# Performance work log

Measured on AMD Instinct MI355X. Metric: run time of the kernel, lower is better.

The kernel has to match this reference:

```python
import jax, jax.numpy as jnp
from jax import lax
import numpy as np

B, N, J, NI, D = 2, 2048, 24, 9, 3
CD, HID = 16, 128
SOFT_BLEND = 20.0
MAX_STEPS, CVG = 50, 1e-5
INIT_BONES = np.array([0, 1, 2, 4, 5, 16, 17, 18, 19])


def _mlp(params, x):
    h = x
    for W, b in params[:-1]:
        h = jax.nn.softplus(h @ W + b)
    W, b = params[-1]
    return h @ W + b


def _broyden(g, x0, J_inv0):
    # x0: [P,3,1], J_inv0: [P,3,3]; fixed MAX_STEPS iterations, track best iterate
    gx = g(x0)
    err0 = jnp.linalg.norm(gx, axis=(1, 2))
    state = (x0, gx, J_inv0, -(J_inv0 @ gx), x0, err0)

    def body(i, st):
        x, gx, Jinv, upd, bx, berr = st
        dx = upd
        x = x + dx
        gx_new = g(x)
        dgx = gx_new - gx
        vT = jnp.swapaxes(dx, -2, -1) @ Jinv            # [P,1,3]
        a = dx - Jinv @ dgx                              # [P,3,1]
        b = vT @ dgx + 1e-6                              # [P,1,1]
        Jinv = Jinv + (a / b) @ vT                       # rank-1 Broyden update
        upd = -(Jinv @ gx_new)
        err = jnp.linalg.norm(gx_new, axis=(1, 2))
        better = err < berr
        bx = jnp.where(better[:, None, None], x, bx)
        berr = jnp.where(better, err, berr)
        return (x, gx_new, Jinv, upd, bx, berr)

    st = lax.fori_loop(0, MAX_STEPS, body, state)
    return st[4], st[5] < CVG


def setup_inputs():
    key = jax.random.key(0)
    ks = jax.random.split(key, 24)
    xd = 0.5 * jax.random.normal(ks[0], (B, N, D), jnp.float32)
    cond_latent = jax.random.normal(ks[1], (B, CD), jnp.float32)
    # near-identity invertible bone transforms
    R = jnp.eye(3, dtype=jnp.float32) + 0.1 * jax.random.normal(ks[2], (B, J, 3, 3), jnp.float32)
    t = 0.1 * jax.random.normal(ks[3], (B, J, 3), jnp.float32)
    tfs = jnp.zeros((B, J, 4, 4), jnp.float32)
    tfs = tfs.at[..., :3, :3].set(R).at[..., :3, 3].set(t).at[..., 3, 3].set(1.0)

    def w(k, fi, fo):
        return jax.random.normal(k, (fi, fo), jnp.float32) / np.sqrt(fi)

    din = D + CD
    inp = dict(xd=xd, cond_latent=cond_latent, tfs=tfs)
    dims_lbs = [(din, HID), (HID, HID), (HID, HID), (HID, J)]
    dims_disp = [(din, HID), (HID, HID), (HID, HID), (HID, D)]
    for i, (fi, fo) in enumerate(dims_lbs):
        inp[f"lbs_w{i}"] = w(ks[4 + i], fi, fo)
        inp[f"lbs_b{i}"] = jnp.zeros((fo,), jnp.float32)
    for i, (fi, fo) in enumerate(dims_disp):
        inp[f"disp_w{i}"] = w(ks[10 + i], fi, fo)
        inp[f"disp_b{i}"] = jnp.zeros((fo,), jnp.float32)
    return inp


def _forward(xd, cond_latent, tfs, lbs, disp):
    P = B * N
    xd_f = xd.reshape(P, D)
    cond_f = jnp.broadcast_to(cond_latent[:, None], (B, N, CD)).reshape(P, CD)
    tfs_f = jnp.broadcast_to(tfs[:, None], (B, N, J, 4, 4)).reshape(P, J, 4, 4)

    # __init: inverse-skin xd with one-hot weights at each init bone -> [P, NI, 3]
    xd_h = jnp.concatenate([xd_f, jnp.ones((P, 1), xd.dtype)], -1)
    xc_init = jnp.einsum('pnij,pj->pni', jnp.linalg.inv(tfs_f[:, INIT_BONES]), xd_h)[..., :3]

    PI = P * NI
    cond_e = jnp.repeat(cond_f, NI, axis=0)       # [PI, CD]
    tfs_e = jnp.repeat(tfs_f, NI, axis=0)         # [PI, J, 4, 4]
    xd_tgt = jnp.repeat(xd_f, NI, axis=0)         # [PI, 3]
    x0 = xc_init.reshape(PI, D)

    def fwd_skin(xc, lbs_p, cond_p, tfs_p):
        w = jax.nn.softmax(SOFT_BLEND * _mlp(lbs_p, jnp.concatenate([xc, cond_p], -1)), -1)
        xh = jnp.concatenate([xc, jnp.ones_like(xc[:, :1])], -1)
        return jnp.einsum('pn,pnij,pj->pi', w, tfs_p, xh)[:, :3]

    def fwd_skin_pt(x, c, t, lbs_p):
        w = jax.nn.softmax(SOFT_BLEND * _mlp(lbs_p, jnp.concatenate([x, c])))
        xh = jnp.concatenate([x, jnp.ones((1,), x.dtype)])
        return jnp.einsum('n,nij,j->i', w, t, xh)[:3]

    def gradient(xc, lbs_p, cond_p, tfs_p):
        # per-point 3x3 Jacobian of forward skinning wrt canonical point
        f = lambda x, c, t: fwd_skin_pt(x, c, t, lbs_p)
        return jax.vmap(jax.jacfwd(f), in_axes=(0, 0, 0))(xc, cond_p, tfs_p)

    # stop-gradient copies for the no-grad broyden search (torch.no_grad block)
    sg = lax.stop_gradient
    lbs_sg = [(sg(W), sg(b)) for W, b in lbs]
    cond_sg, tfs_sg, xdt_sg = sg(cond_e), sg(tfs_e), sg(xd_tgt)

    J_inv0 = jnp.linalg.inv(gradient(sg(x0), lbs_sg, cond_sg, tfs_sg))

    def g_ng(x):  # x: [PI,3,1]
        return (fwd_skin(x[..., 0], lbs_sg, cond_sg, tfs_sg) - xdt_sg)[..., None]

    x_opt, valid = _broyden(g_ng, sg(x0)[..., None], J_inv0)
    xc_opt = sg(x_opt[..., 0])

    # implicit-differentiation correction (eval_mode=False path)
    xd_opt = fwd_skin(xc_opt, lbs, cond_e, tfs_e)
    grad_inv = jnp.linalg.inv(gradient(xc_opt, lbs, cond_e, tfs_e))
    corr = jnp.einsum('pij,pj->pi', -sg(grad_inv), xd_opt - sg(xd_opt))
    xc = xc_opt + corr

    # __query_cano: beta displacement network
    xc = xc + _mlp(disp, jnp.concatenate([xc, cond_e], -1))
    return xc.reshape(B, N, NI, D), valid.reshape(B, N, NI)


def reference(xd, cond_latent, tfs, lbs_w0, lbs_b0, lbs_w1, lbs_b1, lbs_w2, lbs_b2, lbs_w3, lbs_b3, disp_w0, disp_b0, disp_w1, disp_b1, disp_w2, disp_b2, disp_w3, disp_b3):
    lbs = [(lbs_w0, lbs_b0), (lbs_w1, lbs_b1), (lbs_w2, lbs_b2), (lbs_w3, lbs_b3)]
    disp = [(disp_w0, disp_b0), (disp_w1, disp_b1), (disp_w2, disp_b2), (disp_w3, disp_b3)]
    return _forward(xd, cond_latent, tfs, lbs, disp)
```

## Files before the change

### kernel.cpp

```cpp
#include <hip/hip_runtime.h>
#include <math.h>

#define NB 2
#define NN 2048
#define NJ 24
#define NIB 9
#define NCD 16
#define NHID 128
#define NP (NB * NN)
#define NPI (NP * NIB)
#define NBSTRIDE (NN * NIB)
#define SBLEND 20.0f
#define CVG_EPS 1e-5f
#define MAX_STEPS 50
#define N_A 12

#define HSTR 129
#define INSTRD 21
#define LSTR 25

#define WS_BX 4
#define WS_BE (4 + 3 * NPI)
#define WS_META (4 + 4 * NPI)
#define WS_ST (4 + 5 * NPI)

static __device__ __forceinline__ float softplusf(float x) {
    return fmaxf(x, 0.0f) + log1pf(expf(-fabsf(x)));
}
static __device__ __forceinline__ float sigmoidf(float x) {
    return 1.0f / (1.0f + expf(-x));
}
static __device__ __forceinline__ int bone_of(int ib) {
    return (ib < 3) ? ib : ((ib < 5) ? ib + 1 : ib + 11);
}

template <int K>
static __device__ __forceinline__ void mv_acc16(const float* __restrict__ Wp, const float* inrow,
                                                int jb, float* acc) {
#pragma unroll 4
    for (int k = 0; k < K; k++) {
        float h = inrow[k];
        const float* wk = Wp + k * NHID + jb;
#pragma unroll
        for (int jj = 0; jj < 16; jj++) acc[jj] = fmaf(h, wk[jj], acc[jj]);
    }
}

template <int K, int LDIN>
static __device__ __forceinline__ void val_layer(const float* __restrict__ Wp,
                                                 const float* __restrict__ bp,
                                                 const float* inbase, float (*Hs)[HSTR], int r,
                                                 int jb, bool prebar) {
    float acc[16];
#pragma unroll
    for (int jj = 0; jj < 16; jj++) acc[jj] = bp[jb + jj];
    mv_acc16<K>(Wp, inbase + r * LDIN, jb, acc);
    if (prebar) __syncthreads();
#pragma unroll
    for (int jj = 0; jj < 16; jj++) Hs[r][jb + jj] = softplusf(acc[jj]);
    __syncthreads();
}

template <int K, int LDIN>
static __device__ __forceinline__ void jac_layer(const float* __restrict__ Wp,
                                                 const float* __restrict__ bp,
                                                 const float* inbase, float (*Hs)[HSTR], int r,
                                                 int jb, bool prebar) {
    const bool isval = (r < 16);
    const int p = r & 15;
    float acc[16];
#pragma unroll
    for (int jj = 0; jj < 16; jj++) acc[jj] = isval ? bp[jb + jj] : 0.0f;
    mv_acc16<K>(Wp, inbase + r * LDIN, jb, acc);
    if (prebar) __syncthreads();
#pragma unroll
    for (int jj = 0; jj < 16; jj++) Hs[r][jb + jj] = acc[jj];
    __syncthreads();
    float zv[16];
    if (!isval) {
#pragma unroll
        for (int jj = 0; jj < 16; jj++) zv[jj] = Hs[p][jb + jj];
    }
    __syncthreads();
    if (isval) {
#pragma unroll
        for (int jj = 0; jj < 16; jj++) Hs[r][jb + jj] = softplusf(acc[jj]);
    } else {
#pragma unroll
        for (int jj = 0; jj < 16; jj++) Hs[r][jb + jj] = sigmoidf(zv[jj]) * acc[jj];
    }
    __syncthreads();
}

template <bool JAC>
static __device__ __forceinline__ void logit_layer(const float* __restrict__ Wp,
                                                   const float* __restrict__ bp,
                                                   const float* inbase, float (*Lgs)[LSTR], int r,
                                                   int wid) {
    const int jb = wid * 3;
    const bool isval = (!JAC) || (r < 16);
    float acc[3];
#pragma unroll
    for (int jj = 0; jj < 3; jj++) acc[jj] = isval ? bp[jb + jj] : 0.0f;
#pragma unroll 4
    for (int k = 0; k < NHID; k++) {
        float h = inbase[r * HSTR + k];
        const float* wk = Wp + k * NJ + jb;
#pragma unroll
        for (int jj = 0; jj < 3; jj++) acc[jj] = fmaf(h, wk[jj], acc[jj]);
    }
#pragma unroll
    for (int jj = 0; jj < 3; jj++) Lgs[r][jb + jj] = acc[jj];
    __syncthreads();
}

static __device__ __forceinline__ void broyden_step(
    float* sLgRow, const float* sTm, float tx, float ty, float tz,
    float dx0, float dx1, float dx2,
    float& x0_, float& x1_, float& x2_, float& g0, float& g1, float& g2,
    float& Ji0, float& Ji1, float& Ji2, float& Ji3, float& Ji4, float& Ji5,
    float& Ji6, float& Ji7, float& Ji8,
    float& u0, float& u1, float& u2,
    float& bx0, float& bx1, float& bx2, float& berr) {
    float mx = -1e30f;
#pragma unroll
    for (int j = 0; j < NJ; j++) mx = fmaxf(mx, SBLEND * sLgRow[j]);
    float S = 0.0f;
#pragma unroll
    for (int j = 0; j < NJ; j++) {
        float e = expf(SBLEND * sLgRow[j] - mx);
        sLgRow[j] = e;
        S += e;
    }
    const float invS = 1.0f / S;
    float f0 = 0, f1 = 0, f2 = 0;
#pragma unroll
    for (int j = 0; j < NJ; j++) {
        float sj = sLgRow[j] * invS;
        const float* M = &sTm[j * 12];
        f0 += sj * (M[0] * x0_ + M[1] * x1_ + M[2] * x2_ + M[3]);
        f1 += sj * (M[4] * x0_ + M[5] * x1_ + M[6] * x2_ + M[7]);
        f2 += sj * (M[8] * x0_ + M[9] * x1_ + M[10] * x2_ + M[11]);
    }
    float gn0 = f0 - tx, gn1 = f1 - ty, gn2 = f2 - tz;
    float dg0 = gn0 - g0, dg1 = gn1 - g1, dg2 = gn2 - g2;
    float Jd0 = Ji0 * dg0 + Ji1 * dg1 + Ji2 * dg2;
    float Jd1 = Ji3 * dg0 + Ji4 * dg1 + Ji5 * dg2;
    float Jd2 = Ji6 * dg0 + Ji7 * dg1 + Ji8 * dg2;
    float v0 = dx0 * Ji0 + dx1 * Ji3 + dx2 * Ji6;
    float v1 = dx0 * Ji1 + dx1 * Ji4 + dx2 * Ji7;
    float v2 = dx0 * Ji2 + dx1 * Ji5 + dx2 * Ji8;
    float a0 = dx0 - Jd0, a1 = dx1 - Jd1, a2 = dx2 - Jd2;
    float bden = v0 * dg0 + v1 * dg1 + v2 * dg2 + 1e-6f;
    float s0 = a0 / bden, s1 = a1 / bden, s2 = a2 / bden;
    Ji0 += s0 * v0; Ji1 += s0 * v1; Ji2 += s0 * v2;
    Ji3 += s1 * v0; Ji4 += s1 * v1; Ji5 += s1 * v2;
    Ji6 += s2 * v0; Ji7 += s2 * v1; Ji8 += s2 * v2;
    u0 = -(Ji0 * gn0 + Ji1 * gn1 + Ji2 * gn2);
    u1 = -(Ji3 * gn0 + Ji4 * gn1 + Ji5 * gn2);
    u2 = -(Ji6 * gn0 + Ji7 * gn1 + Ji8 * gn2);
    float err = sqrtf(gn0 * gn0 + gn1 * gn1 + gn2 * gn2);
    if (err < berr) { berr = err; bx0 = x0_; bx1 = x1_; bx2 = x2_; }
    g0 = gn0; g1 = gn1; g2 = gn2;
}

__global__ __launch_bounds__(512) void kernel_a(
    const float* __restrict__ xd, const float* __restrict__ cond, const float* __restrict__ tfs,
    const float* __restrict__ lw0, const float* __restrict__ lb0,
    const float* __restrict__ lw1, const float* __restrict__ lb1,
    const float* __restrict__ lw2, const float* __restrict__ lb2,
    const float* __restrict__ lw3, const float* __restrict__ lb3,
    float* __restrict__ ws) {
    __shared__ float sIN[64][INSTRD];
    __shared__ float sH[64][HSTR];
    __shared__ float sLg[64][LSTR];
    __shared__ float sTm[NJ * 12];
    __shared__ int sCnt;

    const int tid = threadIdx.x;
    const int r = tid & 63;
    const int wid = __builtin_amdgcn_readfirstlane(tid >> 6);
    const int jb = wid * 16;
    const int pi0 = blockIdx.x * 64;
    const int b = pi0 / NBSTRIDE;
    const int pi = pi0 + r;

    for (int t = tid; t < NJ * 12; t += 512) {
        int j = t / 12, rc = t % 12;
        sTm[t] = tfs[(size_t)(b * NJ + j) * 16 + rc];
    }
    if (tid >= 16 && tid < 64) {
        const int d = (tid >> 4) - 1;
#pragma unroll
        for (int k = 0; k < 19; k++) sIN[tid][k] = (k == d) ? 1.0f : 0.0f;
    }
    if (tid < 16) {
#pragma unroll
        for (int cc = 0; cc < NCD; cc++) sIN[tid][3 + cc] = cond[b * NCD + cc];
    }

    float x0_ = 0, x1_ = 0, x2_ = 0, g0 = 0, g1 = 0, g2 = 0;
    float Ji0 = 0, Ji1 = 0, Ji2 = 0, Ji3 = 0, Ji4 = 0, Ji5 = 0, Ji6 = 0, Ji7 = 0, Ji8 = 0;
    float u0 = 0, u1 = 0, u2 = 0, bx0 = 0, bx1 = 0, bx2 = 0, berr = 0;
    float tx = 0, ty = 0, tz = 0;
    if (tid < 64) {
        const int pp = pi / NIB;
        tx = xd[pp * 3 + 0]; ty = xd[pp * 3 + 1]; tz = xd[pp * 3 + 2];
    }

#pragma unroll 1
    for (int pass = 0; pass < 4; ++pass) {
        __syncthreads();
        if (tid < 64 && (tid >> 4) == pass) {
            const int p = tid & 15;
            const int ib = pi % NIB;
            const float* T = tfs + (size_t)(b * NJ + bone_of(ib)) * 16;
            float r00 = T[0], r01 = T[1], r02 = T[2], t0 = T[3];
            float r10 = T[4], r11 = T[5], r12 = T[6], t1 = T[7];
            float r20 = T[8], r21 = T[9], r22 = T[10], t2 = T[11];
            float det = r00 * (r11 * r22 - r12 * r21) - r01 * (r10 * r22 - r12 * r20) +
                        r02 * (r10 * r21 - r11 * r20);
            float rd = 1.0f / det;
            float i00 = (r11 * r22 - r12 * r21) * rd, i01 = -(r01 * r22 - r02 * r21) * rd,
                  i02 = (r01 * r12 - r02 * r11) * rd;
            float i10 = -(r10 * r22 - r12 * r20) * rd, i11 = (r00 * r22 - r02 * r20) * rd,
                  i12 = -(r00 * r12 - r02 * r10) * rd;
            float i20 = (r10 * r21 - r11 * r20) * rd, i21 = -(r00 * r21 - r01 * r20) * rd,
                  i22 = (r00 * r11 - r01 * r10) * rd;
            float vx = tx - t0, vy = ty - t1, vz = tz - t2;
            x0_ = i00 * vx + i01 * vy + i02 * vz;
            x1_ = i10 * vx + i11 * vy + i12 * vz;
            x2_ = i20 * vx + i21 * vy + i22 * vz;
            sIN[p][0] = x0_; sIN[p][1] = x1_; sIN[p][2] = x2_;
        }
        __syncthreads();

        jac_layer<19, INSTRD>(lw0, lb0, &sIN[0][0], sH, r, jb, false);
        jac_layer<NHID, HSTR>(lw1, lb1, &sH[0][0], sH, r, jb, true);
        jac_layer<NHID, HSTR>(lw2, lb2, &sH[0][0], sH, r, jb, true);
        logit_layer<true>(lw3, lb3, &sH[0][0], sLg, r, wid);

        if (tid < 64 && (tid >> 4) == pass) {
            const int p = tid & 15;
            float mx = -1e30f;
#pragma unroll
            for (int j = 0; j < NJ; j++) mx = fmaxf(mx, SBLEND * sLg[p][j]);
            float S = 0.0f;
#pragma unroll
            for (int j = 0; j < NJ; j++) S += expf(SBLEND * sLg[p][j] - mx);
            const float invS = 1.0f / S;
            float d0 = 0, d1 = 0, d2 = 0;
#pragma unroll
            for (int j = 0; j < NJ; j++) {
                float sj = expf(SBLEND * sLg[p][j] - mx) * invS;
                d0 += sj * (SBLEND * sLg[16 + p][j]);
                d1 += sj * (SBLEND * sLg[32 + p][j]);
                d2 += sj * (SBLEND * sLg[48 + p][j]);
            }
            float f0 = 0, f1 = 0, f2 = 0;
            float J00 = 0, J01 = 0, J02 = 0, J10 = 0, J11 = 0, J12 = 0, J20 = 0, J21 = 0,
                  J22 = 0;
#pragma unroll
            for (int j = 0; j < NJ; j++) {
                float sj = expf(SBLEND * sLg[p][j] - mx) * invS;
                float uj0 = SBLEND * sLg[16 + p][j], uj1 = SBLEND * sLg[32 + p][j],
                      uj2 = SBLEND * sLg[48 + p][j];
                float sd0 = sj * (uj0 - d0), sd1 = sj * (uj1 - d1), sd2 = sj * (uj2 - d2);
                const float* M = &sTm[j * 12];
                float y0 = M[0] * x0_ + M[1] * x1_ + M[2] * x2_ + M[3];
                float y1 = M[4] * x0_ + M[5] * x1_ + M[6] * x2_ + M[7];
                float y2 = M[8] * x0_ + M[9] * x1_ + M[10] * x2_ + M[11];
                f0 += sj * y0; f1 += sj * y1; f2 += sj * y2;
                J00 += sd0 * y0 + sj * M[0]; J01 += sd1 * y0 + sj * M[1]; J02 += sd2 * y0 + sj * M[2];
                J10 += sd0 * y1 + sj * M[4]; J11 += sd1 * y1 + sj * M[5]; J12 += sd2 * y1 + sj * M[6];
                J20 += sd0 * y2 + sj * M[8]; J21 += sd1 * y2 + sj * M[9]; J22 += sd2 * y2 + sj * M[10];
            }
            g0 = f0 - tx; g1 = f1 - ty; g2 = f2 - tz;
            float detJ = J00 * (J11 * J22 - J12 * J21) - J01 * (J10 * J22 - J12 * J20) +
                         J02 * (J10 * J21 - J11 * J20);
            float rdJ = 1.0f / detJ;
            Ji0 = (J11 * J22 - J12 * J21) * rdJ; Ji1 = -(J01 * J22 - J02 * J21) * rdJ;
            Ji2 = (J01 * J12 - J02 * J11) * rdJ;
            Ji3 = -(J10 * J22 - J12 * J20) * rdJ; Ji4 = (J00 * J22 - J02 * J20) * rdJ;
            Ji5 = -(J00 * J12 - J02 * J10) * rdJ;
            Ji6 = (J10 * J21 - J11 * J20) * rdJ; Ji7 = -(J00 * J21 - J01 * J20) * rdJ;
            Ji8 = (J00 * J11 - J01 * J10) * rdJ;
            u0 = -(Ji0 * g0 + Ji1 * g1 + Ji2 * g2);
            u1 = -(Ji3 * g0 + Ji4 * g1 + Ji5 * g2);
            u2 = -(Ji6 * g0 + Ji7 * g1 + Ji8 * g2);
            berr = sqrtf(g0 * g0 + g1 * g1 + g2 * g2);
            bx0 = x0_; bx1 = x1_; bx2 = x2_;
        }
    }

    if (tid < 64) {
#pragma unroll
        for (int cc = 0; cc < NCD; cc++) sIN[tid][3 + cc] = cond[b * NCD + cc];
    }

    int itdone = 0;
#pragma unroll 1
    for (int it = 0; it < N_A; ++it) {
        float dx0 = 0, dx1 = 0, dx2 = 0;
        if (tid < 64) {
            dx0 = u0; dx1 = u1; dx2 = u2;
            x0_ += dx0; x1_ += dx1; x2_ += dx2;
            sIN[tid][0] = x0_; sIN[tid][1] = x1_; sIN[tid][2] = x2_;
        }
        __syncthreads();

        val_layer<19, INSTRD>(lw0, lb0, &sIN[0][0], sH, r, jb, false);
        val_layer<NHID, HSTR>(lw1, lb1, &sH[0][0], sH, r, jb, true);
        val_layer<NHID, HSTR>(lw2, lb2, &sH[0][0], sH, r, jb, true);
        logit_layer<false>(lw3, lb3, &sH[0][0], sLg, r, wid);

        if (tid < 64) {
            broyden_step(&sLg[r][0], sTm, tx, ty, tz, dx0, dx1, dx2,
                         x0_, x1_, x2_, g0, g1, g2,
                         Ji0, Ji1, Ji2, Ji3, Ji4, Ji5, Ji6, Ji7, Ji8,
                         u0, u1, u2, bx0, bx1, bx2, berr);
            unsigned long long m = __ballot(!(berr < CVG_EPS));
            if (tid == 0) sCnt = (int)__popcll(m);
        }
        __syncthreads();
        itdone = it + 1;
        if (sCnt == 0) break;
    }

    if (tid < 64) {
        ws[WS_BX + pi * 3 + 0] = bx0;
        ws[WS_BX + pi * 3 + 1] = bx1;
        ws[WS_BX + pi * 3 + 2] = bx2;
        ws[WS_BE + pi] = berr;
        const int remaining = MAX_STEPS - itdone;
        if (remaining > 0 && !(berr < CVG_EPS)) {
            int idx = atomicAdd((int*)ws + b, 1);
            int slot = b * NBSTRIDE + idx;
            ((int*)ws)[WS_META + slot] = pi | (remaining << 20);
            float st[15] = {x0_, x1_, x2_, g0, g1, g2, Ji0, Ji1, Ji2, Ji3, Ji4, Ji5, Ji6, Ji7, Ji8};
#pragma unroll
            for (int c = 0; c < 15; c++) ws[WS_ST + c * NPI + slot] = st[c];
        }
    }
}

__global__ __launch_bounds__(512) void kernel_b(
    const float* __restrict__ xd, const float* __restrict__ cond, const float* __restrict__ tfs,
    const float* __restrict__ lw0, const float* __restrict__ lb0,
    const float* __restrict__ lw1, const float* __restrict__ lb1,
    const float* __restrict__ lw2, const float* __restrict__ lb2,
    const float* __restrict__ lw3, const float* __restrict__ lb3,
    float* __restrict__ ws) {
    const int bid = blockIdx.x;
    const int batch = (bid < 288) ? 0 : 1;
    const int chunk0 = (bid - batch * 288) * 64;
    const int S = ((const int*)ws)[batch];
    if (chunk0 >= S) return;

    __shared__ float sIN[64][INSTRD];
    __shared__ float sH[64][HSTR];
    __shared__ float sLg[64][LSTR];
    __shared__ float sTm[NJ * 12];
    __shared__ int sCnt;

    const int tid = threadIdx.x;
    const int r = tid & 63;
    const int wid = __builtin_amdgcn_readfirstlane(tid >> 6);
    const int jb = wid * 16;

    for (int t = tid; t < NJ * 12; t += 512) {
        int j = t / 12, rc = t % 12;
        sTm[t] = tfs[(size_t)(batch * NJ + j) * 16 + rc];
    }

    float x0_ = 0, x1_ = 0, x2_ = 0, g0 = 0, g1 = 0, g2 = 0;
    float Ji0 = 1, Ji1 = 0, Ji2 = 0, Ji3 = 0, Ji4 = 1, Ji5 = 0, Ji6 = 0, Ji7 = 0, Ji8 = 1;
    float u0 = 0, u1 = 0, u2 = 0, bx0 = 0, bx1 = 0, bx2 = 0, berr = 0;
    float tx = 0, ty = 0, tz = 0;
    int pi = -1, itleft = 0;
    bool realrow = false;
    if (tid < 64) {
        const int k = chunk0 + r;
        realrow = (k < S);
        if (realrow) {
            const int slot = batch * NBSTRIDE + k;
            const int meta = ((const int*)ws)[WS_META + slot];
            pi = meta & 0xFFFFF;
            itleft = meta >> 20;
            x0_ = ws[WS_ST + 0 * NPI + slot]; x1_ = ws[WS_ST + 1 * NPI + slot];
            x2_ = ws[WS_ST + 2 * NPI + slot];
            g0 = ws[WS_ST + 3 * NPI + slot]; g1 = ws[WS_ST + 4 * NPI + slot];
            g2 = ws[WS_ST + 5 * NPI + slot];
            Ji0 = ws[WS_ST + 6 * NPI + slot]; Ji1 = ws[WS_ST + 7 * NPI + slot];
            Ji2 = ws[WS_ST + 8 * NPI + slot];
            Ji3 = ws[WS_ST + 9 * NPI + slot]; Ji4 = ws[WS_ST + 10 * NPI + slot];
            Ji5 = ws[WS_ST + 11 * NPI + slot];
            Ji6 = ws[WS_ST + 12 * NPI + slot]; Ji7 = ws[WS_ST + 13 * NPI + slot];
            Ji8 = ws[WS_ST + 14 * NPI + slot];
            u0 = -(Ji0 * g0 + Ji1 * g1 + Ji2 * g2);
            u1 = -(Ji3 * g0 + Ji4 * g1 + Ji5 * g2);
            u2 = -(Ji6 * g0 + Ji7 * g1 + Ji8 * g2);
            bx0 = ws[WS_BX + pi * 3 + 0]; bx1 = ws[WS_BX + pi * 3 + 1];
            bx2 = ws[WS_BX + pi * 3 + 2];
            berr = ws[WS_BE + pi];
            const int pp = pi / NIB;
            tx = xd[pp * 3 + 0]; ty = xd[pp * 3 + 1]; tz = xd[pp * 3 + 2];
        }
#pragma unroll
        for (int cc = 0; cc < NCD; cc++) sIN[tid][3 + cc] = cond[batch * NCD + cc];
        sIN[tid][0] = 0; sIN[tid][1] = 0; sIN[tid][2] = 0;
    }

#pragma unroll 1
    for (int it = 0; it < MAX_STEPS; ++it) {
        bool active = false;
        float dx0 = 0, dx1 = 0, dx2 = 0;
        if (tid < 64) {
            active = realrow && (itleft > 0) && !(berr < CVG_EPS);
            if (active) {
                dx0 = u0; dx1 = u1; dx2 = u2;
                x0_ += dx0; x1_ += dx1; x2_ += dx2;
            }
            sIN[tid][0] = x0_; sIN[tid][1] = x1_; sIN[tid][2] = x2_;
        }
        __syncthreads();

        val_layer<19, INSTRD>(lw0, lb0, &sIN[0][0], sH, r, jb, false);
        val_layer<NHID, HSTR>(lw1, lb1, &sH[0][0], sH, r, jb, true);
        val_layer<NHID, HSTR>(lw2, lb2, &sH[0][0], sH, r, jb, true);
        logit_layer<false>(lw3, lb3, &sH[0][0], sLg, r, wid);

        if (tid < 64) {
            if (active) {
                broyden_step(&sLg[r][0], sTm, tx, ty, tz, dx0, dx1, dx2,
                             x0_, x1_, x2_, g0, g1, g2,
                             Ji0, Ji1, Ji2, Ji3, Ji4, Ji5, Ji6, Ji7, Ji8,
                             u0, u1, u2, bx0, bx1, bx2, berr);
                itleft--;
            }
            unsigned long long m =
                __ballot(realrow && (itleft > 0) && !(berr < CVG_EPS));
            if (tid == 0) sCnt = (int)__popcll(m);
        }
        __syncthreads();
        if (sCnt == 0) break;
    }

    if (tid < 64 && realrow) {
        ws[WS_BX + pi * 3 + 0] = bx0;
        ws[WS_BX + pi * 3 + 1] = bx1;
        ws[WS_BX + pi * 3 + 2] = bx2;
        ws[WS_BE + pi] = berr;
    }
}

__global__ __launch_bounds__(512) void kernel_c(
    const float* __restrict__ cond,
    const float* __restrict__ dw0, const float* __restrict__ db0,
    const float* __restrict__ dw1, const float* __restrict__ db1,
    const float* __restrict__ dw2, const float* __restrict__ db2,
    const float* __restrict__ dw3, const float* __restrict__ db3,
    const float* __restrict__ ws, float* __restrict__ out) {
    __shared__ float sIN[64][INSTRD];
    __shared__ float sH[64][HSTR];

    const int tid = threadIdx.x;
    const int r = tid & 63;
    const int wid = __builtin_amdgcn_readfirstlane(tid >> 6);
    const int jb = wid * 16;
    const int pi0 = blockIdx.x * 64;
    const int b = pi0 / NBSTRIDE;
    const int pi = pi0 + r;

    float bx0 = 0, bx1 = 0, bx2 = 0, berr = 0;
    if (tid < 64) {
        bx0 = ws[WS_BX + pi * 3 + 0]; bx1 = ws[WS_BX + pi * 3 + 1];
        bx2 = ws[WS_BX + pi * 3 + 2];
        berr = ws[WS_BE + pi];
        sIN[tid][0] = bx0; sIN[tid][1] = bx1; sIN[tid][2] = bx2;
#pragma unroll
        for (int cc = 0; cc < NCD; cc++) sIN[tid][3 + cc] = cond[b * NCD + cc];
    }
    __syncthreads();

    val_layer<19, INSTRD>(dw0, db0, &sIN[0][0], sH, r, jb, false);
    val_layer<NHID, HSTR>(dw1, db1, &sH[0][0], sH, r, jb, true);
    val_layer<NHID, HSTR>(dw2, db2, &sH[0][0], sH, r, jb, true);

    if (tid < 64) {
        float a0 = db3[0], a1 = db3[1], a2 = db3[2];
#pragma unroll 4
        for (int k = 0; k < NHID; k++) {
            float h = sH[tid][k];
            a0 = fmaf(h, dw3[k * 3 + 0], a0);
            a1 = fmaf(h, dw3[k * 3 + 1], a1);
            a2 = fmaf(h, dw3[k * 3 + 2], a2);
        }
        out[pi * 3 + 0] = bx0 + a0;
        out[pi * 3 + 1] = bx1 + a1;
        out[pi * 3 + 2] = bx2 + a2;
        out[3 * NPI + pi] = (berr < CVG_EPS) ? 1.0f : 0.0f;
    }
}

extern "C" void kernel_launch(void* const* d_in, const int* in_sizes, int n_in,
                              void* d_out, int out_size, void* d_ws, size_t ws_size,
                              hipStream_t stream) {
    (void)in_sizes; (void)n_in; (void)out_size; (void)ws_size;
    const float* xd   = (const float*)d_in[0];
    const float* cond = (const float*)d_in[1];
    const float* tfs  = (const float*)d_in[2];
    const float* lw0 = (const float*)d_in[3];  const float* lb0 = (const float*)d_in[4];
    const float* lw1 = (const float*)d_in[5];  const float* lb1 = (const float*)d_in[6];
    const float* lw2 = (const float*)d_in[7];  const float* lb2 = (const float*)d_in[8];
    const float* lw3 = (const float*)d_in[9];  const float* lb3 = (const float*)d_in[10];
    const float* dw0 = (const float*)d_in[11]; const float* db0 = (const float*)d_in[12];
    const float* dw1 = (const float*)d_in[13]; const float* db1 = (const float*)d_in[14];
    const float* dw2 = (const float*)d_in[15]; const float* db2 = (const float*)d_in[16];
    const float* dw3 = (const float*)d_in[17]; const float* db3 = (const float*)d_in[18];
    float* ws = (float*)d_ws;
    float* out = (float*)d_out;

    hipMemsetAsync(d_ws, 0, 16, stream);
    kernel_a<<<NPI / 64, 512, 0, stream>>>(xd, cond, tfs, lw0, lb0, lw1, lb1, lw2, lb2,
                                           lw3, lb3, ws);
    kernel_b<<<576, 512, 0, stream>>>(xd, cond, tfs, lw0, lb0, lw1, lb1, lw2, lb2,
                                      lw3, lb3, ws);
    kernel_c<<<NPI / 64, 512, 0, stream>>>(cond, dw0, db0, dw1, db1, dw2, db2, dw3, db3,
                                           ws, out);
}
```

Before: 1.244 ms.

## Replicate Broyden state across all warps and replace block barrier with wave-level vote

Every one of the 8 waves now runs the per-row Broyden update redundantly on its own registers, instead of only wave 0 doing it. This lets each wave decide loop exit with a wave-local __all vote, removing the shared counter, ballot and extra __syncthreads per iteration. The softmax now recomputes the exps instead of writing them back to shared memory, which avoids write races between the replicated waves. The cost is duplicated ALU work (expf for 24 bones, 3x3 updates) in every wave. It also relies on all waves reaching the same exit decision so the remaining block barriers stay matched.

```diff
diff --git a/kernel.cpp b/kernel.cpp
--- a/kernel.cpp
+++ b/kernel.cpp
@@ -15,6 +15,8 @@
 #define MAX_STEPS 50
 #define N_A 12
 
+#define ROWS 64
+#define NTHR 512
 #define HSTR 129
 #define INSTRD 21
 #define LSTR 25
@@ -35,8 +37,8 @@
 }
 
 template <int K>
-static __device__ __forceinline__ void mv_acc16(const float* __restrict__ Wp, const float* inrow,
-                                                int jb, float* acc) {
+static __device__ __forceinline__ void mv_acc16(const float* __restrict__ Wp,
+                                                const float* inrow, int jb, float* acc) {
 #pragma unroll 4
     for (int k = 0; k < K; k++) {
         float h = inrow[k];
@@ -49,8 +51,8 @@
 template <int K, int LDIN>
 static __device__ __forceinline__ void val_layer(const float* __restrict__ Wp,
                                                  const float* __restrict__ bp,
-                                                 const float* inbase, float (*Hs)[HSTR], int r,
-                                                 int jb, bool prebar) {
+                                                 const float* inbase, float (*Hs)[HSTR],
+                                                 int r, int jb, bool prebar) {
     float acc[16];
 #pragma unroll
     for (int jj = 0; jj < 16; jj++) acc[jj] = bp[jb + jj];
@@ -64,8 +66,8 @@
 template <int K, int LDIN>
 static __device__ __forceinline__ void jac_layer(const float* __restrict__ Wp,
                                                  const float* __restrict__ bp,
-                                                 const float* inbase, float (*Hs)[HSTR], int r,
-                                                 int jb, bool prebar) {
+                                                 const float* inbase, float (*Hs)[HSTR],
+                                                 int r, int jb, bool prebar) {
     const bool isval = (r < 16);
     const int p = r & 15;
     float acc[16];
@@ -77,7 +79,7 @@
     for (int jj = 0; jj < 16; jj++) Hs[r][jb + jj] = acc[jj];
     __syncthreads();
     float zv[16];
-    if (!isval) {
+    {
 #pragma unroll
         for (int jj = 0; jj < 16; jj++) zv[jj] = Hs[p][jb + jj];
     }
@@ -95,8 +97,8 @@
 template <bool JAC>
 static __device__ __forceinline__ void logit_layer(const float* __restrict__ Wp,
                                                    const float* __restrict__ bp,
-                                                   const float* inbase, float (*Lgs)[LSTR], int r,
-                                                   int wid) {
+                                                   const float* inbase, float (*Lgs)[LSTR],
+                                                   int r, int wid) {
     const int jb = wid * 3;
     const bool isval = (!JAC) || (r < 16);
     float acc[3];
@@ -114,8 +116,8 @@
     __syncthreads();
 }
 
-static __device__ __forceinline__ void broyden_step(
-    float* sLgRow, const float* sTm, float tx, float ty, float tz,
+static __device__ __forceinline__ void broyden_step_rep(
+    const float* sLgRow, const float* sTm, float tx, float ty, float tz,
     float dx0, float dx1, float dx2,
     float& x0_, float& x1_, float& x2_, float& g0, float& g1, float& g2,
     float& Ji0, float& Ji1, float& Ji2, float& Ji3, float& Ji4, float& Ji5,
@@ -127,16 +129,12 @@
     for (int j = 0; j < NJ; j++) mx = fmaxf(mx, SBLEND * sLgRow[j]);
     float S = 0.0f;
 #pragma unroll
-    for (int j = 0; j < NJ; j++) {
-        float e = expf(SBLEND * sLgRow[j] - mx);
-        sLgRow[j] = e;
-        S += e;
-    }
+    for (int j = 0; j < NJ; j++) S += expf(SBLEND * sLgRow[j] - mx);
     const float invS = 1.0f / S;
     float f0 = 0, f1 = 0, f2 = 0;
 #pragma unroll
     for (int j = 0; j < NJ; j++) {
-        float sj = sLgRow[j] * invS;
+        float sj = expf(SBLEND * sLgRow[j] - mx) * invS;
         const float* M = &sTm[j * 12];
         f0 += sj * (M[0] * x0_ + M[1] * x1_ + M[2] * x2_ + M[3]);
         f1 += sj * (M[4] * x0_ + M[5] * x1_ + M[6] * x2_ + M[7]);
@@ -164,28 +162,27 @@
     g0 = gn0; g1 = gn1; g2 = gn2;
 }
 
-__global__ __launch_bounds__(512) void kernel_a(
+__global__ __launch_bounds__(NTHR) void kernel_a(
     const float* __restrict__ xd, const float* __restrict__ cond, const float* __restrict__ tfs,
     const float* __restrict__ lw0, const float* __restrict__ lb0,
     const float* __restrict__ lw1, const float* __restrict__ lb1,
     const float* __restrict__ lw2, const float* __restrict__ lb2,
     const float* __restrict__ lw3, const float* __restrict__ lb3,
     float* __restrict__ ws) {
-    __shared__ float sIN[64][INSTRD];
-    __shared__ float sH[64][HSTR];
-    __shared__ float sLg[64][LSTR];
+    __shared__ float sIN[ROWS][INSTRD];
+    __shared__ float sH[ROWS][HSTR];
+    __shared__ float sLg[ROWS][LSTR];
     __shared__ float sTm[NJ * 12];
-    __shared__ int sCnt;
 
     const int tid = threadIdx.x;
     const int r = tid & 63;
     const int wid = __builtin_amdgcn_readfirstlane(tid >> 6);
     const int jb = wid * 16;
-    const int pi0 = blockIdx.x * 64;
+    const int pi0 = blockIdx.x * ROWS;
     const int b = pi0 / NBSTRIDE;
     const int pi = pi0 + r;
 
-    for (int t = tid; t < NJ * 12; t += 512) {
+    for (int t = tid; t < NJ * 12; t += NTHR) {
         int j = t / 12, rc = t % 12;
         sTm[t] = tfs[(size_t)(b * NJ + j) * 16 + rc];
     }
@@ -202,17 +199,13 @@
     float x0_ = 0, x1_ = 0, x2_ = 0, g0 = 0, g1 = 0, g2 = 0;
     float Ji0 = 0, Ji1 = 0, Ji2 = 0, Ji3 = 0, Ji4 = 0, Ji5 = 0, Ji6 = 0, Ji7 = 0, Ji8 = 0;
     float u0 = 0, u1 = 0, u2 = 0, bx0 = 0, bx1 = 0, bx2 = 0, berr = 0;
-    float tx = 0, ty = 0, tz = 0;
-    if (tid < 64) {
-        const int pp = pi / NIB;
-        tx = xd[pp * 3 + 0]; ty = xd[pp * 3 + 1]; tz = xd[pp * 3 + 2];
-    }
+    const int pp = pi / NIB;
+    const float tx = xd[pp * 3 + 0], ty = xd[pp * 3 + 1], tz = xd[pp * 3 + 2];
 
 #pragma unroll 1
     for (int pass = 0; pass < 4; ++pass) {
-        __syncthreads();
-        if (tid < 64 && (tid >> 4) == pass) {
-            const int p = tid & 15;
+        if ((r >> 4) == pass) {
+            const int p = r & 15;
             const int ib = pi % NIB;
             const float* T = tfs + (size_t)(b * NJ + bone_of(ib)) * 16;
             float r00 = T[0], r01 = T[1], r02 = T[2], t0 = T[3];
@@ -240,8 +233,8 @@
         jac_layer<NHID, HSTR>(lw2, lb2, &sH[0][0], sH, r, jb, true);
         logit_layer<true>(lw3, lb3, &sH[0][0], sLg, r, wid);
 
-        if (tid < 64 && (tid >> 4) == pass) {
-            const int p = tid & 15;
+        if ((r >> 4) == pass) {
+            const int p = r & 15;
             float mx = -1e30f;
 #pragma unroll
             for (int j = 0; j < NJ; j++) mx = fmaxf(mx, SBLEND * sLg[p][j]);
@@ -293,20 +286,15 @@
         }
     }
 
-    if (tid < 64) {
-#pragma unroll
-        for (int cc = 0; cc < NCD; cc++) sIN[tid][3 + cc] = cond[b * NCD + cc];
-    }
+#pragma unroll
+    for (int cc = 0; cc < NCD; cc++) sIN[r][3 + cc] = cond[b * NCD + cc];
 
     int itdone = 0;
 #pragma unroll 1
     for (int it = 0; it < N_A; ++it) {
-        float dx0 = 0, dx1 = 0, dx2 = 0;
-        if (tid < 64) {
-            dx0 = u0; dx1 = u1; dx2 = u2;
-            x0_ += dx0; x1_ += dx1; x2_ += dx2;
-            sIN[tid][0] = x0_; sIN[tid][1] = x1_; sIN[tid][2] = x2_;
-        }
+        float dx0 = u0, dx1 = u1, dx2 = u2;
+        x0_ += dx0; x1_ += dx1; x2_ += dx2;
+        sIN[r][0] = x0_; sIN[r][1] = x1_; sIN[r][2] = x2_;
         __syncthreads();
 
         val_layer<19, INSTRD>(lw0, lb0, &sIN[0][0], sH, r, jb, false);
@@ -314,17 +302,12 @@
         val_layer<NHID, HSTR>(lw2, lb2, &sH[0][0], sH, r, jb, true);
         logit_layer<false>(lw3, lb3, &sH[0][0], sLg, r, wid);
 
-        if (tid < 64) {
-            broyden_step(&sLg[r][0], sTm, tx, ty, tz, dx0, dx1, dx2,
+        broyden_step_rep(&sLg[r][0], sTm, tx, ty, tz, dx0, dx1, dx2,
                          x0_, x1_, x2_, g0, g1, g2,
                          Ji0, Ji1, Ji2, Ji3, Ji4, Ji5, Ji6, Ji7, Ji8,
                          u0, u1, u2, bx0, bx1, bx2, berr);
-            unsigned long long m = __ballot(!(berr < CVG_EPS));
-            if (tid == 0) sCnt = (int)__popcll(m);
-        }
-        __syncthreads();
         itdone = it + 1;
-        if (sCnt == 0) break;
+        if (__all(berr < CVG_EPS)) break;
     }
 
     if (tid < 64) {
@@ -344,7 +327,7 @@
     }
 }
 
-__global__ __launch_bounds__(512) void kernel_b(
+__global__ __launch_bounds__(NTHR) void kernel_b(
     const float* __restrict__ xd, const float* __restrict__ cond, const float* __restrict__ tfs,
     const float* __restrict__ lw0, const float* __restrict__ lb0,
     const float* __restrict__ lw1, const float* __restrict__ lb1,
@@ -353,22 +336,21 @@
     float* __restrict__ ws) {
     const int bid = blockIdx.x;
     const int batch = (bid < 288) ? 0 : 1;
-    const int chunk0 = (bid - batch * 288) * 64;
+    const int chunk0 = (bid - batch * 288) * ROWS;
     const int S = ((const int*)ws)[batch];
     if (chunk0 >= S) return;
 
-    __shared__ float sIN[64][INSTRD];
-    __shared__ float sH[64][HSTR];
-    __shared__ float sLg[64][LSTR];
+    __shared__ float sIN[ROWS][INSTRD];
+    __shared__ float sH[ROWS][HSTR];
+    __shared__ float sLg[ROWS][LSTR];
     __shared__ float sTm[NJ * 12];
-    __shared__ int sCnt;
 
     const int tid = threadIdx.x;
     const int r = tid & 63;
     const int wid = __builtin_amdgcn_readfirstlane(tid >> 6);
     const int jb = wid * 16;
 
-    for (int t = tid; t < NJ * 12; t += 512) {
+    for (int t = tid; t < NJ * 12; t += NTHR) {
         int j = t / 12, rc = t % 12;
         sTm[t] = tfs[(size_t)(batch * NJ + j) * 16 + rc];
     }
@@ -378,51 +360,43 @@
     float u0 = 0, u1 = 0, u2 = 0, bx0 = 0, bx1 = 0, bx2 = 0, berr = 0;
     float tx = 0, ty = 0, tz = 0;
     int pi = -1, itleft = 0;
-    bool realrow = false;
-    if (tid < 64) {
-        const int k = chunk0 + r;
-        realrow = (k < S);
-        if (realrow) {
-            const int slot = batch * NBSTRIDE + k;
-            const int meta = ((const int*)ws)[WS_META + slot];
-            pi = meta & 0xFFFFF;
-            itleft = meta >> 20;
-            x0_ = ws[WS_ST + 0 * NPI + slot]; x1_ = ws[WS_ST + 1 * NPI + slot];
-            x2_ = ws[WS_ST + 2 * NPI + slot];
-            g0 = ws[WS_ST + 3 * NPI + slot]; g1 = ws[WS_ST + 4 * NPI + slot];
-            g2 = ws[WS_ST + 5 * NPI + slot];
-            Ji0 = ws[WS_ST + 6 * NPI + slot]; Ji1 = ws[WS_ST + 7 * NPI + slot];
-            Ji2 = ws[WS_ST + 8 * NPI + slot];
-            Ji3 = ws[WS_ST + 9 * NPI + slot]; Ji4 = ws[WS_ST + 10 * NPI + slot];
-            Ji5 = ws[WS_ST + 11 * NPI + slot];
-            Ji6 = ws[WS_ST + 12 * NPI + slot]; Ji7 = ws[WS_ST + 13 * NPI + slot];
-            Ji8 = ws[WS_ST + 14 * NPI + slot];
-            u0 = -(Ji0 * g0 + Ji1 * g1 + Ji2 * g2);
-            u1 = -(Ji3 * g0 + Ji4 * g1 + Ji5 * g2);
-            u2 = -(Ji6 * g0 + Ji7 * g1 + Ji8 * g2);
-            bx0 = ws[WS_BX + pi * 3 + 0]; bx1 = ws[WS_BX + pi * 3 + 1];
-            bx2 = ws[WS_BX + pi * 3 + 2];
-            berr = ws[WS_BE + pi];
-            const int pp = pi / NIB;
-            tx = xd[pp * 3 + 0]; ty = xd[pp * 3 + 1]; tz = xd[pp * 3 + 2];
-        }
-#pragma unroll
-        for (int cc = 0; cc < NCD; cc++) sIN[tid][3 + cc] = cond[batch * NCD + cc];
-        sIN[tid][0] = 0; sIN[tid][1] = 0; sIN[tid][2] = 0;
-    }
+    const bool realrow = (chunk0 + r < S);
+    if (realrow) {
+        const int slot = batch * NBSTRIDE + chunk0 + r;
+        const int meta = ((const int*)ws)[WS_META + slot];
+        pi = meta & 0xFFFFF;
+        itleft = meta >> 20;
+        x0_ = ws[WS_ST + 0 * NPI + slot]; x1_ = ws[WS_ST + 1 * NPI + slot];
+        x2_ = ws[WS_ST + 2 * NPI + slot];
+        g0 = ws[WS_ST + 3 * NPI + slot]; g1 = ws[WS_ST + 4 * NPI + slot];
+        g2 = ws[WS_ST + 5 * NPI + slot];
+        Ji0 = ws[WS_ST + 6 * NPI + slot]; Ji1 = ws[WS_ST + 7 * NPI + slot];
+        Ji2 = ws[WS_ST + 8 * NPI + slot];
+        Ji3 = ws[WS_ST + 9 * NPI + slot]; Ji4 = ws[WS_ST + 10 * NPI + slot];
+        Ji5 = ws[WS_ST + 11 * NPI + slot];
+        Ji6 = ws[WS_ST + 12 * NPI + slot]; Ji7 = ws[WS_ST + 13 * NPI + slot];
+        Ji8 = ws[WS_ST + 14 * NPI + slot];
+        u0 = -(Ji0 * g0 + Ji1 * g1 + Ji2 * g2);
+        u1 = -(Ji3 * g0 + Ji4 * g1 + Ji5 * g2);
+        u2 = -(Ji6 * g0 + Ji7 * g1 + Ji8 * g2);
+        bx0 = ws[WS_BX + pi * 3 + 0]; bx1 = ws[WS_BX + pi * 3 + 1];
+        bx2 = ws[WS_BX + pi * 3 + 2];
+        berr = ws[WS_BE + pi];
+        const int pp = pi / NIB;
+        tx = xd[pp * 3 + 0]; ty = xd[pp * 3 + 1]; tz = xd[pp * 3 + 2];
+    }
+#pragma unroll
+    for (int cc = 0; cc < NCD; cc++) sIN[r][3 + cc] = cond[batch * NCD + cc];
 
 #pragma unroll 1
     for (int it = 0; it < MAX_STEPS; ++it) {
-        bool active = false;
+        bool active = realrow && (itleft > 0) && !(berr < CVG_EPS);
         float dx0 = 0, dx1 = 0, dx2 = 0;
-        if (tid < 64) {
-            active = realrow && (itleft > 0) && !(berr < CVG_EPS);
-            if (active) {
-                dx0 = u0; dx1 = u1; dx2 = u2;
-                x0_ += dx0; x1_ += dx1; x2_ += dx2;
-            }
-            sIN[tid][0] = x0_; sIN[tid][1] = x1_; sIN[tid][2] = x2_;
+        if (active) {
+            dx0 = u0; dx1 = u1; dx2 = u2;
+            x0_ += dx0; x1_ += dx1; x2_ += dx2;
         }
+        sIN[r][0] = x0_; sIN[r][1] = x1_; sIN[r][2] = x2_;
         __syncthreads();
 
         val_layer<19, INSTRD>(lw0, lb0, &sIN[0][0], sH, r, jb, false);
@@ -430,20 +404,14 @@
         val_layer<NHID, HSTR>(lw2, lb2, &sH[0][0], sH, r, jb, true);
         logit_layer<false>(lw3, lb3, &sH[0][0], sLg, r, wid);
 
-        if (tid < 64) {
-            if (active) {
-                broyden_step(&sLg[r][0], sTm, tx, ty, tz, dx0, dx1, dx2,
+        if (active) {
+            broyden_step_rep(&sLg[r][0], sTm, tx, ty, tz, dx0, dx1, dx2,
                              x0_, x1_, x2_, g0, g1, g2,
                              Ji0, Ji1, Ji2, Ji3, Ji4, Ji5, Ji6, Ji7, Ji8,
                              u0, u1, u2, bx0, bx1, bx2, berr);
-                itleft--;
-            }
-            unsigned long long m =
-                __ballot(realrow && (itleft > 0) && !(berr < CVG_EPS));
-            if (tid == 0) sCnt = (int)__popcll(m);
+            itleft--;
         }
-        __syncthreads();
-        if (sCnt == 0) break;
+        if (__all(!(realrow && (itleft > 0) && !(berr < CVG_EPS)))) break;
     }
 
     if (tid < 64 && realrow) {
@@ -454,48 +422,46 @@
     }
 }
 
-__global__ __launch_bounds__(512) void kernel_c(
+__global__ __launch_bounds__(NTHR) void kernel_c(
     const float* __restrict__ cond,
     const float* __restrict__ dw0, const float* __restrict__ db0,
     const float* __restrict__ dw1, const float* __restrict__ db1,
     const float* __restrict__ dw2, const float* __restrict__ db2,
     const float* __restrict__ dw3, const float* __restrict__ db3,
     const float* __restrict__ ws, float* __restrict__ out) {
-    __shared__ float sIN[64][INSTRD];
-    __shared__ float sH[64][HSTR];
+    __shared__ float sIN[ROWS][INSTRD];
+    __shared__ float sH[ROWS][HSTR];
 
     const int tid = threadIdx.x;
     const int r = tid & 63;
     const int wid = __builtin_amdgcn_readfirstlane(tid >> 6);
     const int jb = wid * 16;
-    const int pi0 = blockIdx.x * 64;
+    const int pi0 = blockIdx.x * ROWS;
     const int b = pi0 / NBSTRIDE;
     const int pi = pi0 + r;
 
-    float bx0 = 0, bx1 = 0, bx2 = 0, berr = 0;
-    if (tid < 64) {
-        bx0 = ws[WS_BX + pi * 3 + 0]; bx1 = ws[WS_BX + pi * 3 + 1];
-        bx2 = ws[WS_BX + pi * 3 + 2];
-        berr = ws[WS_BE + pi];
-        sIN[tid][0] = bx0; sIN[tid][1] = bx1; sIN[tid][2] = bx2;
-#pragma unroll
-        for (int cc = 0; cc < NCD; cc++) sIN[tid][3 + cc] = cond[b * NCD + cc];
-    }
+    const float bx0 = ws[WS_BX + pi * 3 + 0];
+    const float bx1 = ws[WS_BX + pi * 3 + 1];
+    const float bx2 = ws[WS_BX + pi * 3 + 2];
+    const float berr = ws[WS_BE + pi];
+    sIN[r][0] = bx0; sIN[r][1] = bx1; sIN[r][2] = bx2;
+#pragma unroll
+    for (int cc = 0; cc < NCD; cc++) sIN[r][3 + cc] = cond[b * NCD + cc];
     __syncthreads();
 
     val_layer<19, INSTRD>(dw0, db0, &sIN[0][0], sH, r, jb, false);
     val_layer<NHID, HSTR>(dw1, db1, &sH[0][0], sH, r, jb, true);
     val_layer<NHID, HSTR>(dw2, db2, &sH[0][0], sH, r, jb, true);
 
+    float a0 = db3[0], a1 = db3[1], a2 = db3[2];
+#pragma unroll 4
+    for (int k = 0; k < NHID; k++) {
+        float h = sH[r][k];
+        a0 = fmaf(h, dw3[k * 3 + 0], a0);
+        a1 = fmaf(h, dw3[k * 3 + 1], a1);
+        a2 = fmaf(h, dw3[k * 3 + 2], a2);
+    }
     if (tid < 64) {
-        float a0 = db3[0], a1 = db3[1], a2 = db3[2];
-#pragma unroll 4
-        for (int k = 0; k < NHID; k++) {
-            float h = sH[tid][k];
-            a0 = fmaf(h, dw3[k * 3 + 0], a0);
-            a1 = fmaf(h, dw3[k * 3 + 1], a1);
-            a2 = fmaf(h, dw3[k * 3 + 2], a2);
-        }
         out[pi * 3 + 0] = bx0 + a0;
         out[pi * 3 + 1] = bx1 + a1;
         out[pi * 3 + 2] = bx2 + a2;
@@ -522,10 +488,10 @@
     float* out = (float*)d_out;
 
     hipMemsetAsync(d_ws, 0, 16, stream);
-    kernel_a<<<NPI / 64, 512, 0, stream>>>(xd, cond, tfs, lw0, lb0, lw1, lb1, lw2, lb2,
-                                           lw3, lb3, ws);
-    kernel_b<<<576, 512, 0, stream>>>(xd, cond, tfs, lw0, lb0, lw1, lb1, lw2, lb2,
-                                      lw3, lb3, ws);
-    kernel_c<<<NPI / 64, 512, 0, stream>>>(cond, dw0, db0, dw1, db1, dw2, db2, dw3, db3,
-                                           ws, out);
-}
+    kernel_a<<<NPI / ROWS, NTHR, 0, stream>>>(xd, cond, tfs, lw0, lb0, lw1, lb1, lw2, lb2,
+                                              lw3, lb3, ws);
+    kernel_b<<<576, NTHR, 0, stream>>>(xd, cond, tfs, lw0, lb0, lw1, lb1, lw2, lb2,
+                                       lw3, lb3, ws);
+    kernel_c<<<NPI / ROWS, NTHR, 0, stream>>>(cond, dw0, db0, dw1, db1, dw2, db2, dw3, db3,
+                                              ws, out);
+}
```

Result: slower. 1.520 ms (+22.1%).
